# Kernel tuning notes

Hardware: AMD Instinct MI355X
Metric: run time of the kernel (lower is better)

The kernel has to match this reference:

```python
import jax, jax.numpy as jnp
import numpy as np

B, S, H, E = 2, 4096, 2048, 8


def setup_inputs() -> dict:
    key = jax.random.key(0)
    k1, k2, k3 = jax.random.split(key, 3)
    x = jax.random.normal(k1, (B, S, H), dtype=jnp.float32)
    w_router = jax.random.normal(k2, (E, H), dtype=jnp.float32) * (1.0 / np.sqrt(H))
    # nn.Linear weight layout: [out_features, in_features] per expert -> [E, H, H]
    w_experts = jax.random.normal(k3, (E, H, H), dtype=jnp.float32) * (1.0 / np.sqrt(H))
    return {"x": x, "w_router": w_router, "w_experts": w_experts}


def reference(x, w_router, w_experts):
    # router logits: x @ W_r^T  -> [B, S, E]
    logits = jnp.einsum('bsh,eh->bse', x, w_router)
    idx = jnp.argmax(logits, axis=-1)  # [B, S] top-1 expert per token
    # dense all-expert outputs (matches original which evaluates every expert):
    # expert_e(x) = x @ W_e^T -> [B, S, E, H]
    all_out = jnp.einsum('bsh,efh->bsef', x, w_experts)
    # masked sum over one-hot mask == gather of the selected expert output
    out = jnp.take_along_axis(all_out, idx[:, :, None, None], axis=2)[:, :, 0, :]
    return out
```

## Files before the change

### kernel.cpp

```cpp
#include <hip/hip_runtime.h>
#include <hip/hip_bf16.h>
#include <cstdint>

#define T_TOK 8192
#define H_DIM 2048
#define N_EXP 8
#define FLAGBIT 0x80000000u

typedef __attribute__((ext_vector_type(4))) float f32x4;
typedef __attribute__((ext_vector_type(8))) short bf16x8;

__device__ __forceinline__ unsigned short f2bf(float f) {
  unsigned int u = __builtin_bit_cast(unsigned int, f);
  u += 0x7fffu + ((u >> 16) & 1u);
  return (unsigned short)(u >> 16);
}

#define GLL(SRC, DST) __builtin_amdgcn_global_load_lds( \
    (const __attribute__((address_space(1))) void*)(SRC), \
    (__attribute__((address_space(3))) void*)(DST), 16, 0, 0)

__global__ __launch_bounds__(256, 4) void k_conv(const float* __restrict__ we,
                                                 unsigned short* __restrict__ wb) {
  const size_t tix = ((size_t)blockIdx.x * 256 + threadIdx.x) * 8;
  const size_t stride = (size_t)2048 * 256 * 8;
  f32x4 v[16];
#pragma unroll
  for (int it = 0; it < 8; ++it) {
    v[2 * it]     = *reinterpret_cast<const f32x4*>(we + tix + (size_t)it * stride);
    v[2 * it + 1] = *reinterpret_cast<const f32x4*>(we + tix + (size_t)it * stride + 4);
  }
#pragma unroll
  for (int it = 0; it < 8; ++it) {
    union { unsigned short h[8]; uint4 u; } r;
#pragma unroll
    for (int q = 0; q < 4; ++q) {
      r.h[q]     = f2bf(v[2 * it][q]);
      r.h[4 + q] = f2bf(v[2 * it + 1][q]);
    }
    *reinterpret_cast<uint4*>(wb + tix + (size_t)it * stride) = r.u;
  }
}

__global__ __launch_bounds__(256) void k_router(const float* __restrict__ x,
    const float* __restrict__ wr, unsigned short* __restrict__ xb,
    int* __restrict__ idx)
{
  const int wv = threadIdx.x >> 6, lane = threadIdx.x & 63;
  const int t0 = (blockIdx.x * 4 + wv) * 4;
  float acc[4][N_EXP];
#pragma unroll
  for (int tt = 0; tt < 4; ++tt)
#pragma unroll
    for (int e = 0; e < N_EXP; ++e) acc[tt][e] = 0.f;
#pragma unroll
  for (int c = 0; c < H_DIM / 256; ++c) {
    const int h = c * 256 + lane * 4;
    float4 wvv[N_EXP];
#pragma unroll
    for (int e = 0; e < N_EXP; ++e)
      wvv[e] = *reinterpret_cast<const float4*>(wr + e * H_DIM + h);
#pragma unroll
    for (int tt = 0; tt < 4; ++tt) {
      const float4 xv = *reinterpret_cast<const float4*>(x + (size_t)(t0 + tt) * H_DIM + h);
      ushort4 bv;
      bv.x = f2bf(xv.x); bv.y = f2bf(xv.y); bv.z = f2bf(xv.z); bv.w = f2bf(xv.w);
      *reinterpret_cast<ushort4*>(xb + (size_t)(t0 + tt) * H_DIM + h) = bv;
#pragma unroll
      for (int e = 0; e < N_EXP; ++e) {
        acc[tt][e] = fmaf(xv.x, wvv[e].x, acc[tt][e]);
        acc[tt][e] = fmaf(xv.y, wvv[e].y, acc[tt][e]);
        acc[tt][e] = fmaf(xv.z, wvv[e].z, acc[tt][e]);
        acc[tt][e] = fmaf(xv.w, wvv[e].w, acc[tt][e]);
      }
    }
  }
#pragma unroll
  for (int off = 32; off >= 1; off >>= 1)
#pragma unroll
    for (int tt = 0; tt < 4; ++tt)
#pragma unroll
      for (int e = 0; e < N_EXP; ++e) acc[tt][e] += __shfl_xor(acc[tt][e], off, 64);
  if (lane == 0) {
#pragma unroll
    for (int tt = 0; tt < 4; ++tt) {
      float best = acc[tt][0]; int be = 0;
#pragma unroll
      for (int e = 1; e < N_EXP; ++e) if (acc[tt][e] > best) { best = acc[tt][e]; be = e; }
      idx[t0 + tt] = be;
    }
  }
}

__global__ __launch_bounds__(256) void k_hist(const int* __restrict__ idx,
                                              int* __restrict__ hist)
{
  __shared__ int wc[4][N_EXP];
  const int b = blockIdx.x, w = threadIdx.x >> 6, l = threadIdx.x & 63;
  const int e = idx[b * 256 + threadIdx.x];
#pragma unroll
  for (int ee = 0; ee < N_EXP; ++ee) {
    const unsigned long long bm = __ballot(e == ee);
    if (l == ee) wc[w][ee] = __popcll(bm);
  }
  __syncthreads();
  if (threadIdx.x < N_EXP)
    hist[b * N_EXP + threadIdx.x] = wc[0][threadIdx.x] + wc[1][threadIdx.x]
                                  + wc[2][threadIdx.x] + wc[3][threadIdx.x];
}

__global__ void k_scan(const int* __restrict__ hist, int* __restrict__ boff,
                       int* __restrict__ estar, int* __restrict__ mlo, int* __restrict__ mhi,
                       int* __restrict__ rpos, int* __restrict__ rtile, int* __restrict__ rtc)
{
  __shared__ int sC[N_EXP], sE[32], sCnt[N_EXP], sBase[N_EXP];
  const int lane = threadIdx.x;
  if (lane < N_EXP) {
    int s = 0;
    for (int b = 0; b < 32; ++b) s += hist[b * N_EXP + lane];
    sC[lane] = s;
  }
  __syncthreads();
  int off[N_EXP + 1]; off[0] = 0;
#pragma unroll
  for (int e = 0; e < N_EXP; ++e) off[e + 1] = off[e] + sC[e];
  if (lane < 32) {
    for (int e = 0; e < N_EXP; ++e) {
      int s = off[e];
      for (int b = 0; b < lane; ++b) s += hist[b * N_EXP + e];
      boff[lane * N_EXP + e] = s;
    }
    const int lo = lane * 256, hi = lo + 256;
    int bl = -1, bE = 0, bLo = 0, bHi = 0;
#pragma unroll
    for (int e = 0; e < N_EXP; ++e) {
      const int a = off[e] > lo ? off[e] : lo;
      const int b = off[e + 1] < hi ? off[e + 1] : hi;
      if (b - a > bl) { bl = b - a; bE = e; bLo = a - lo; bHi = b - lo; }
    }
    sE[lane] = bE; estar[lane] = bE; mlo[lane] = bLo; mhi[lane] = bHi;
  }
  __syncthreads();
  if (lane < N_EXP) {
    int cnt = 0;
    for (int t = 0; t < 32; ++t) {
      if (sE[t] == lane) continue;
      const int lo = t * 256, hi = lo + 256;
      const int a = off[lane] > lo ? off[lane] : lo;
      const int b = off[lane + 1] < hi ? off[lane + 1] : hi;
      if (b > a) cnt += b - a;
    }
    sCnt[lane] = cnt;
  }
  __syncthreads();
  if (lane == 0) {
    int base = 0, ntile = 0;
    for (int e = 0; e < N_EXP; ++e) {
      sBase[e] = base;
      const int pt = (sCnt[e] + 127) >> 7;
      for (int k = 0; k < pt; ++k) rtile[ntile++] = e;
      base += pt << 7;
    }
    *rtc = ntile;
  }
  __syncthreads();
  if (lane < N_EXP && sCnt[lane] > 0) {
    int ptr = sBase[lane], firstp = -1;
    for (int t = 0; t < 32; ++t) {
      if (sE[t] == lane) continue;
      const int lo = t * 256, hi = lo + 256;
      const int a = off[lane] > lo ? off[lane] : lo;
      const int b = off[lane + 1] < hi ? off[lane + 1] : hi;
      for (int p = a; p < b; ++p) { if (firstp < 0) firstp = p; rpos[ptr++] = p; }
    }
    const int end = sBase[lane] + (((sCnt[lane] + 127) >> 7) << 7);
    for (; ptr < end; ++ptr) rpos[ptr] = (int)((unsigned)firstp | FLAGBIT);
  }
}

__global__ __launch_bounds__(256) void k_place(const int* __restrict__ idx,
    const int* __restrict__ boff, int* __restrict__ tlist)
{
  __shared__ int wc[4][N_EXP];
  const int b = blockIdx.x, w = threadIdx.x >> 6, l = threadIdx.x & 63;
  const int t = b * 256 + threadIdx.x;
  const int e = idx[t];
  int rank = 0;
#pragma unroll
  for (int ee = 0; ee < N_EXP; ++ee) {
    const unsigned long long bm = __ballot(e == ee);
    if (e == ee) rank = __popcll(bm & ((1ull << l) - 1ull));
    if (l == ee) wc[w][ee] = __popcll(bm);
  }
  __syncthreads();
  int pre = 0;
  for (int ww = 0; ww < 4; ++ww) if (ww < w) pre += wc[ww][e];
  tlist[boff[b * N_EXP + e] + pre + rank] = t;
}

template<int Q, bool LOADB, bool VMC>
__device__ __forceinline__ void gphase(const char* LP,
    __attribute__((address_space(3))) char* LDS3,
    int rdBase, int aRowOff, int bRowOff, int ch0, int ch1,
    bf16x8 (&bfr)[8], f32x4 (&acc)[8][4],
    const unsigned short* s0, const unsigned short* s1, int d0, int d1)
{
  if constexpr (LOADB) {
#pragma unroll
    for (int nf = 0; nf < 4; ++nf) {
      bfr[nf * 2 + 0] = *reinterpret_cast<const bf16x8*>(LP + rdBase + 32768 + bRowOff + nf * 2048 + ch0);
      bfr[nf * 2 + 1] = *reinterpret_cast<const bf16x8*>(LP + rdBase + 32768 + bRowOff + nf * 2048 + ch1);
    }
  }
  bf16x8 af[2][2];
#pragma unroll
  for (int m = 0; m < 2; ++m) {
    af[m][0] = *reinterpret_cast<const bf16x8*>(LP + rdBase + aRowOff + (2 * Q + m) * 2048 + ch0);
    af[m][1] = *reinterpret_cast<const bf16x8*>(LP + rdBase + aRowOff + (2 * Q + m) * 2048 + ch1);
  }
  GLL(s0, LDS3 + d0);
  GLL(s1, LDS3 + d1);
  __builtin_amdgcn_sched_barrier(0);
  __builtin_amdgcn_s_barrier();
  __builtin_amdgcn_sched_barrier(0);
  __builtin_amdgcn_s_setprio(1);
#pragma unroll
  for (int ks = 0; ks < 2; ++ks)
#pragma unroll
    for (int m = 0; m < 2; ++m)
#pragma unroll
      for (int nf = 0; nf < 4; ++nf)
        acc[2 * Q + m][nf] = __builtin_amdgcn_mfma_f32_16x16x32_bf16(af[m][ks], bfr[nf * 2 + ks], acc[2 * Q + m][nf], 0, 0, 0);
  __builtin_amdgcn_s_setprio(0);
  if constexpr (VMC) asm volatile("s_waitcnt vmcnt(4)" ::: "memory");
  __builtin_amdgcn_sched_barrier(0);
  __builtin_amdgcn_s_barrier();
  __builtin_amdgcn_sched_barrier(0);
}

__global__ __launch_bounds__(512, 2) void k_gemm(const unsigned short* __restrict__ xb,
    const unsigned short* __restrict__ wb, const int* __restrict__ tlist,
    const int* __restrict__ estar, const int* __restrict__ mlo, const int* __restrict__ mhi,
    float* __restrict__ out)
{
  __shared__ short lds[65536];
  const int bid = blockIdx.x;
  const int mt = (bid & 7) * 4 + ((bid >> 3) & 3);
  const int nt = bid >> 5;
  const int m0 = mt * 256, f0 = nt * 256;
  const int e = estar[mt], mLo = mlo[mt], mHi = mhi[mt];
  const int tid = threadIdx.x;
  const int l = tid & 63, wv = tid >> 6;
  const int wm = wv >> 2, wn = wv & 3;
  const int l16 = l & 15, g = l >> 4;
  const char* LP = (const char*)lds;
  auto* LDS3 = (__attribute__((address_space(3))) char*)lds;

  const int sw = l16 & 7;
  const int ch0 = ((0 + g) ^ sw) << 4;
  const int ch1 = ((4 + g) ^ sw) << 4;
  const int aRowOff = (wm * 128 + l16) * 128;
  const int bRowOff = (wn * 64 + l16) * 128;

  const int csrc = ((l & 7) ^ ((l >> 3) & 7)) * 8;
  const int srow = l >> 3;
  const unsigned short* aP[2][2];
  const unsigned short* bP[2][2];
  const unsigned short* wpan = wb + (size_t)e * H_DIM * H_DIM;
#pragma unroll
  for (int h = 0; h < 2; ++h)
#pragma unroll
    for (int j = 0; j < 2; ++j) {
      const int tok = tlist[m0 + h * 128 + (wv * 2 + j) * 8 + srow];
      aP[h][j] = xb + (size_t)tok * H_DIM + csrc;
      bP[h][j] = wpan + (size_t)(f0 + h * 128 + (wv * 2 + j) * 8 + srow) * H_DIM + csrc;
    }
  const int sl0 = wv * 2048, sl1 = wv * 2048 + 1024;

  f32x4 acc[8][4];
#pragma unroll
  for (int mf = 0; mf < 8; ++mf)
#pragma unroll
    for (int nf = 0; nf < 4; ++nf) acc[mf][nf] = (f32x4){0.f, 0.f, 0.f, 0.f};
  bf16x8 bfr[8];

  GLL(aP[0][0], LDS3 + 0 + sl0);      GLL(aP[0][1], LDS3 + 0 + sl1);
  GLL(aP[1][0], LDS3 + 16384 + sl0);  GLL(aP[1][1], LDS3 + 16384 + sl1);
  GLL(bP[0][0], LDS3 + 32768 + sl0);  GLL(bP[0][1], LDS3 + 32768 + sl1);
  GLL(bP[1][0], LDS3 + 49152 + sl0);  GLL(bP[1][1], LDS3 + 49152 + sl1);
  GLL(bP[0][0] + 64, LDS3 + 65536 + 32768 + sl0);  GLL(bP[0][1] + 64, LDS3 + 65536 + 32768 + sl1);
  GLL(bP[1][0] + 64, LDS3 + 65536 + 49152 + sl0);  GLL(bP[1][1] + 64, LDS3 + 65536 + 49152 + sl1);
  asm volatile("s_waitcnt vmcnt(4)" ::: "memory");
  __builtin_amdgcn_sched_barrier(0);
  __builtin_amdgcn_s_barrier();
  __builtin_amdgcn_sched_barrier(0);

  for (int i = 0; i < 16; ++i) {
    const int kk1 = ((2 * i + 1) << 6) & (H_DIM - 1);
    const int kk2 = ((2 * i + 2) << 6) & (H_DIM - 1);
    const int kk3 = ((2 * i + 3) << 6) & (H_DIM - 1);
    gphase<0, true , false>(LP, LDS3, 0, aRowOff, bRowOff, ch0, ch1, bfr, acc,
        aP[0][0] + kk1, aP[0][1] + kk1, 65536 + 0 + sl0, 65536 + 0 + sl1);
    gphase<1, false, false>(LP, LDS3, 0, aRowOff, bRowOff, ch0, ch1, bfr, acc,
        aP[1][0] + kk1, aP[1][1] + kk1, 65536 + 16384 + sl0, 65536 + 16384 + sl1);
    gphase<2, false, false>(LP, LDS3, 0, aRowOff, bRowOff, ch0, ch1, bfr, acc,
        bP[0][0] + kk2, bP[0][1] + kk2, 0 + 32768 + sl0, 0 + 32768 + sl1);
    gphase<3, false, true >(LP, LDS3, 0, aRowOff, bRowOff, ch0, ch1, bfr, acc,
        bP[1][0] + kk2, bP[1][1] + kk2, 0 + 49152 + sl0, 0 + 49152 + sl1);
    gphase<0, true , false>(LP, LDS3, 65536, aRowOff, bRowOff, ch0, ch1, bfr, acc,
        aP[0][0] + kk2, aP[0][1] + kk2, 0 + 0 + sl0, 0 + 0 + sl1);
    gphase<1, false, false>(LP, LDS3, 65536, aRowOff, bRowOff, ch0, ch1, bfr, acc,
        aP[1][0] + kk2, aP[1][1] + kk2, 0 + 16384 + sl0, 0 + 16384 + sl1);
    gphase<2, false, false>(LP, LDS3, 65536, aRowOff, bRowOff, ch0, ch1, bfr, acc,
        bP[0][0] + kk3, bP[0][1] + kk3, 65536 + 32768 + sl0, 65536 + 32768 + sl1);
    gphase<3, false, true >(LP, LDS3, 65536, aRowOff, bRowOff, ch0, ch1, bfr, acc,
        bP[1][0] + kk3, bP[1][1] + kk3, 65536 + 49152 + sl0, 65536 + 49152 + sl1);
  }

#pragma unroll
  for (int mf = 0; mf < 8; ++mf) {
#pragma unroll
    for (int r = 0; r < 4; ++r) {
      const int row = wm * 128 + mf * 16 + g * 4 + r;
      const int t = tlist[m0 + row];
      const bool own = (row >= mLo) && (row < mHi);
      float* op = out + (size_t)t * H_DIM + f0 + wn * 64 + l16;
#pragma unroll
      for (int nf = 0; nf < 4; ++nf) op[nf * 16] = own ? acc[mf][nf][r] : 0.f;
    }
  }
}

__global__ __launch_bounds__(256, 2) void k_repair(const unsigned short* __restrict__ xb,
    const unsigned short* __restrict__ wb, const int* __restrict__ tlist,
    const int* __restrict__ rpos, const int* __restrict__ rtile, const int* __restrict__ rtc,
    float* __restrict__ out)
{
  const int bx = blockIdx.x;
  if (bx >= *rtc) return;
  __shared__ short lds[24576];
  const int f0 = blockIdx.y * 256, kc = blockIdx.z;
  const int e = rtile[bx];
  const int tid = threadIdx.x, l = tid & 63, wv = tid >> 6;
  const int wm = wv >> 1, wn = wv & 1;
  const int l16 = l & 15, g = l >> 4;
  const char* LP = (const char*)lds;
  auto* LDS3 = (__attribute__((address_space(3))) char*)lds;
  const int sw = l16 & 7;
  const int ch0 = ((0 + g) ^ sw) << 4, ch1 = ((4 + g) ^ sw) << 4;
  const int csrc = ((l & 7) ^ ((l >> 3) & 7)) * 8;
  const int srow = l >> 3;

  const unsigned short* aS[4];
#pragma unroll
  for (int j = 0; j < 4; ++j) {
    const int ent = rpos[bx * 128 + (wv * 4 + j) * 8 + srow];
    const int tok = tlist[ent & 0x7fffffff];
    aS[j] = xb + (size_t)tok * H_DIM + csrc;
  }
  const unsigned short* bS[8];
#pragma unroll
  for (int j = 0; j < 8; ++j)
    bS[j] = wb + (size_t)e * H_DIM * H_DIM + (size_t)(f0 + (wv * 8 + j) * 8 + srow) * H_DIM + csrc;

  f32x4 acc[4][8];
#pragma unroll
  for (int mf = 0; mf < 4; ++mf)
#pragma unroll
    for (int nf = 0; nf < 8; ++nf) acc[mf][nf] = (f32x4){0.f, 0.f, 0.f, 0.f};

  for (int it = 0; it < 8; ++it) {
    const int kk = kc * 512 + it * 64;
    __syncthreads();
#pragma unroll
    for (int j = 0; j < 4; ++j) GLL(aS[j] + kk, LDS3 + (wv * 4 + j) * 1024);
#pragma unroll
    for (int j = 0; j < 8; ++j) GLL(bS[j] + kk, LDS3 + 16384 + (wv * 8 + j) * 1024);
    __syncthreads();
    bf16x8 af[4][2];
#pragma unroll
    for (int mf = 0; mf < 4; ++mf) {
      af[mf][0] = *reinterpret_cast<const bf16x8*>(LP + (wm * 64 + mf * 16 + l16) * 128 + ch0);
      af[mf][1] = *reinterpret_cast<const bf16x8*>(LP + (wm * 64 + mf * 16 + l16) * 128 + ch1);
    }
#pragma unroll
    for (int nf = 0; nf < 8; ++nf) {
      const bf16x8 b0 = *reinterpret_cast<const bf16x8*>(LP + 16384 + (wn * 128 + nf * 16 + l16) * 128 + ch0);
      const bf16x8 b1 = *reinterpret_cast<const bf16x8*>(LP + 16384 + (wn * 128 + nf * 16 + l16) * 128 + ch1);
#pragma unroll
      for (int mf = 0; mf < 4; ++mf) {
        acc[mf][nf] = __builtin_amdgcn_mfma_f32_16x16x32_bf16(af[mf][0], b0, acc[mf][nf], 0, 0, 0);
        acc[mf][nf] = __builtin_amdgcn_mfma_f32_16x16x32_bf16(af[mf][1], b1, acc[mf][nf], 0, 0, 0);
      }
    }
  }
#pragma unroll
  for (int mf = 0; mf < 4; ++mf) {
#pragma unroll
    for (int r = 0; r < 4; ++r) {
      const int row = wm * 64 + mf * 16 + g * 4 + r;
      const int ent = rpos[bx * 128 + row];
      if (!((unsigned)ent & FLAGBIT)) {
        const int tok = tlist[ent];
        float* op = out + (size_t)tok * H_DIM + f0 + wn * 128 + l16;
#pragma unroll
        for (int nf = 0; nf < 8; ++nf) atomicAdd(op + nf * 16, acc[mf][nf][r]);
      }
    }
  }
}

extern "C" void kernel_launch(void* const* d_in, const int* in_sizes, int n_in,
                              void* d_out, int out_size, void* d_ws, size_t ws_size,
                              hipStream_t stream) {
  const float* x  = (const float*)d_in[0];
  const float* wr = (const float*)d_in[1];
  const float* we = (const float*)d_in[2];
  float* out = (float*)d_out;

  char* p = (char*)d_ws;
  unsigned short* xb = (unsigned short*)p; p += (size_t)T_TOK * H_DIM * 2;
  unsigned short* wb = (unsigned short*)p; p += (size_t)N_EXP * H_DIM * H_DIM * 2;
  int* idx    = (int*)p; p += T_TOK * 4;
  int* tlist  = (int*)p; p += T_TOK * 4;
  int* rpos   = (int*)p; p += T_TOK * 4;
  int* hist   = (int*)p; p += 32 * N_EXP * 4;
  int* boff   = (int*)p; p += 32 * N_EXP * 4;
  int* estar  = (int*)p; p += 32 * 4;
  int* mlo    = (int*)p; p += 32 * 4;
  int* mhi    = (int*)p; p += 32 * 4;
  int* rtile  = (int*)p; p += 64 * 4;
  int* rtc    = (int*)p; p += 64;

  k_conv<<<2048, 256, 0, stream>>>(we, wb);
  k_router<<<512, 256, 0, stream>>>(x, wr, xb, idx);
  k_hist<<<32, 256, 0, stream>>>(idx, hist);
  k_scan<<<1, 64, 0, stream>>>(hist, boff, estar, mlo, mhi, rpos, rtile, rtc);
  k_place<<<32, 256, 0, stream>>>(idx, boff, tlist);
  k_gemm<<<256, 512, 0, stream>>>(xb, wb, tlist, estar, mlo, mhi, out);
  k_repair<<<dim3(64, 8, 4), 256, 0, stream>>>(xb, wb, tlist, rpos, rtile, rtc, out);
}
```

Measured before the change: 209.8 us.

## Fuse hist/scan/place into one sort kernel and split weight conversion

Replaces the three small routing kernels (histogram, scan, placement) with a single 1024-thread block that counts per-wave expert ballots, prefix-sums in shared memory, and scatters token indices directly. This removes two kernel launches and the global round trips through the hist/boff buffers. The fp32-to-bf16 weight conversion is split into two half-size launches, one of which issues loads and stores per iteration instead of batching them, and the router gets a min-blocks launch bound. The single-block sort runs serially on one CU, and the extra conversion launch adds overhead.

```diff
diff --git a/kernel.cpp b/kernel.cpp
--- a/kernel.cpp
+++ b/kernel.cpp
@@ -20,10 +20,10 @@
     (const __attribute__((address_space(1))) void*)(SRC), \
     (__attribute__((address_space(3))) void*)(DST), 16, 0, 0)
 
-__global__ __launch_bounds__(256, 4) void k_conv(const float* __restrict__ we,
-                                                 unsigned short* __restrict__ wb) {
+__global__ __launch_bounds__(256, 4) void k_conv_a(const float* __restrict__ we,
+                                                   unsigned short* __restrict__ wb) {
   const size_t tix = ((size_t)blockIdx.x * 256 + threadIdx.x) * 8;
-  const size_t stride = (size_t)2048 * 256 * 8;
+  const size_t stride = (size_t)1024 * 256 * 8;
   f32x4 v[16];
 #pragma unroll
   for (int it = 0; it < 8; ++it) {
@@ -42,7 +42,22 @@
   }
 }
 
-__global__ __launch_bounds__(256) void k_router(const float* __restrict__ x,
+__global__ __launch_bounds__(256, 4) void k_conv_b(const float* __restrict__ we,
+                                                   unsigned short* __restrict__ wb) {
+  const size_t tix = ((size_t)blockIdx.x * 256 + threadIdx.x) * 8;
+  const size_t stride = (size_t)1024 * 256 * 8;
+#pragma unroll
+  for (int it = 0; it < 8; ++it) {
+    const f32x4 a = *reinterpret_cast<const f32x4*>(we + tix + (size_t)it * stride);
+    const f32x4 b = *reinterpret_cast<const f32x4*>(we + tix + (size_t)it * stride + 4);
+    union { unsigned short h[8]; uint4 u; } r;
+#pragma unroll
+    for (int q = 0; q < 4; ++q) { r.h[q] = f2bf(a[q]); r.h[4 + q] = f2bf(b[q]); }
+    *reinterpret_cast<uint4*>(wb + tix + (size_t)it * stride) = r.u;
+  }
+}
+
+__global__ __launch_bounds__(256, 2) void k_router(const float* __restrict__ x,
     const float* __restrict__ wr, unsigned short* __restrict__ xb,
     int* __restrict__ idx)
 {
@@ -92,45 +107,51 @@
   }
 }
 
-__global__ __launch_bounds__(256) void k_hist(const int* __restrict__ idx,
-                                              int* __restrict__ hist)
+__global__ __launch_bounds__(1024) void k_sort(const int* __restrict__ idx,
+    int* __restrict__ tlist, int* __restrict__ estar, int* __restrict__ mlo,
+    int* __restrict__ mhi, int* __restrict__ rpos, int* __restrict__ rtile,
+    int* __restrict__ rtc)
 {
-  __shared__ int wc[4][N_EXP];
-  const int b = blockIdx.x, w = threadIdx.x >> 6, l = threadIdx.x & 63;
-  const int e = idx[b * 256 + threadIdx.x];
-#pragma unroll
-  for (int ee = 0; ee < N_EXP; ++ee) {
-    const unsigned long long bm = __ballot(e == ee);
-    if (l == ee) wc[w][ee] = __popcll(bm);
-  }
-  __syncthreads();
-  if (threadIdx.x < N_EXP)
-    hist[b * N_EXP + threadIdx.x] = wc[0][threadIdx.x] + wc[1][threadIdx.x]
-                                  + wc[2][threadIdx.x] + wc[3][threadIdx.x];
-}
-
-__global__ void k_scan(const int* __restrict__ hist, int* __restrict__ boff,
-                       int* __restrict__ estar, int* __restrict__ mlo, int* __restrict__ mhi,
-                       int* __restrict__ rpos, int* __restrict__ rtile, int* __restrict__ rtc)
-{
-  __shared__ int sC[N_EXP], sE[32], sCnt[N_EXP], sBase[N_EXP];
-  const int lane = threadIdx.x;
-  if (lane < N_EXP) {
+  __shared__ int wc[N_EXP][128];
+  __shared__ int wbase[N_EXP][128];
+  __shared__ int sTot[N_EXP];
+  __shared__ int off[N_EXP + 1];
+  __shared__ int sE[32], sCnt[N_EXP], sBase[N_EXP];
+  const int tid = threadIdx.x, w = tid >> 6, l = tid & 63;
+  int myE[8];
+#pragma unroll
+  for (int j = 0; j < 8; ++j) {
+    myE[j] = idx[j * 1024 + tid];
+#pragma unroll
+    for (int e = 0; e < N_EXP; ++e) {
+      const unsigned long long bm = __ballot(myE[j] == e);
+      if (l == e) wc[e][j * 16 + w] = __popcll(bm);
+    }
+  }
+  __syncthreads();
+  if (tid < N_EXP) {
     int s = 0;
-    for (int b = 0; b < 32; ++b) s += hist[b * N_EXP + lane];
-    sC[lane] = s;
-  }
-  __syncthreads();
-  int off[N_EXP + 1]; off[0] = 0;
-#pragma unroll
-  for (int e = 0; e < N_EXP; ++e) off[e + 1] = off[e] + sC[e];
-  if (lane < 32) {
+    for (int k = 0; k < 128; ++k) { wbase[tid][k] = s; s += wc[tid][k]; }
+    sTot[tid] = s;
+  }
+  __syncthreads();
+  if (tid == 0) {
+    off[0] = 0;
+    for (int e = 0; e < N_EXP; ++e) off[e + 1] = off[e] + sTot[e];
+  }
+  __syncthreads();
+#pragma unroll
+  for (int j = 0; j < 8; ++j) {
+    int rank = 0;
+#pragma unroll
     for (int e = 0; e < N_EXP; ++e) {
-      int s = off[e];
-      for (int b = 0; b < lane; ++b) s += hist[b * N_EXP + e];
-      boff[lane * N_EXP + e] = s;
-    }
-    const int lo = lane * 256, hi = lo + 256;
+      const unsigned long long bm = __ballot(myE[j] == e);
+      if (myE[j] == e) rank = __popcll(bm & ((1ull << l) - 1ull));
+    }
+    tlist[off[myE[j]] + wbase[myE[j]][j * 16 + w] + rank] = j * 1024 + tid;
+  }
+  if (tid < 32) {
+    const int lo = tid * 256, hi = lo + 256;
     int bl = -1, bE = 0, bLo = 0, bHi = 0;
 #pragma unroll
     for (int e = 0; e < N_EXP; ++e) {
@@ -138,22 +159,22 @@
       const int b = off[e + 1] < hi ? off[e + 1] : hi;
       if (b - a > bl) { bl = b - a; bE = e; bLo = a - lo; bHi = b - lo; }
     }
-    sE[lane] = bE; estar[lane] = bE; mlo[lane] = bLo; mhi[lane] = bHi;
-  }
-  __syncthreads();
-  if (lane < N_EXP) {
+    sE[tid] = bE; estar[tid] = bE; mlo[tid] = bLo; mhi[tid] = bHi;
+  }
+  __syncthreads();
+  if (tid < N_EXP) {
     int cnt = 0;
     for (int t = 0; t < 32; ++t) {
-      if (sE[t] == lane) continue;
+      if (sE[t] == tid) continue;
       const int lo = t * 256, hi = lo + 256;
-      const int a = off[lane] > lo ? off[lane] : lo;
-      const int b = off[lane + 1] < hi ? off[lane + 1] : hi;
+      const int a = off[tid] > lo ? off[tid] : lo;
+      const int b = off[tid + 1] < hi ? off[tid + 1] : hi;
       if (b > a) cnt += b - a;
     }
-    sCnt[lane] = cnt;
-  }
-  __syncthreads();
-  if (lane == 0) {
+    sCnt[tid] = cnt;
+  }
+  __syncthreads();
+  if (tid == 0) {
     int base = 0, ntile = 0;
     for (int e = 0; e < N_EXP; ++e) {
       sBase[e] = base;
@@ -164,38 +185,18 @@
     *rtc = ntile;
   }
   __syncthreads();
-  if (lane < N_EXP && sCnt[lane] > 0) {
-    int ptr = sBase[lane], firstp = -1;
+  if (tid < N_EXP && sCnt[tid] > 0) {
+    int ptr = sBase[tid], firstp = -1;
     for (int t = 0; t < 32; ++t) {
-      if (sE[t] == lane) continue;
+      if (sE[t] == tid) continue;
       const int lo = t * 256, hi = lo + 256;
-      const int a = off[lane] > lo ? off[lane] : lo;
-      const int b = off[lane + 1] < hi ? off[lane + 1] : hi;
+      const int a = off[tid] > lo ? off[tid] : lo;
+      const int b = off[tid + 1] < hi ? off[tid + 1] : hi;
       for (int p = a; p < b; ++p) { if (firstp < 0) firstp = p; rpos[ptr++] = p; }
     }
-    const int end = sBase[lane] + (((sCnt[lane] + 127) >> 7) << 7);
+    const int end = sBase[tid] + (((sCnt[tid] + 127) >> 7) << 7);
     for (; ptr < end; ++ptr) rpos[ptr] = (int)((unsigned)firstp | FLAGBIT);
   }
-}
-
-__global__ __launch_bounds__(256) void k_place(const int* __restrict__ idx,
-    const int* __restrict__ boff, int* __restrict__ tlist)
-{
-  __shared__ int wc[4][N_EXP];
-  const int b = blockIdx.x, w = threadIdx.x >> 6, l = threadIdx.x & 63;
-  const int t = b * 256 + threadIdx.x;
-  const int e = idx[t];
-  int rank = 0;
-#pragma unroll
-  for (int ee = 0; ee < N_EXP; ++ee) {
-    const unsigned long long bm = __ballot(e == ee);
-    if (e == ee) rank = __popcll(bm & ((1ull << l) - 1ull));
-    if (l == ee) wc[w][ee] = __popcll(bm);
-  }
-  __syncthreads();
-  int pre = 0;
-  for (int ww = 0; ww < 4; ++ww) if (ww < w) pre += wc[ww][e];
-  tlist[boff[b * N_EXP + e] + pre + rank] = t;
 }
 
 template<int Q, bool LOADB, bool VMC>
@@ -424,19 +425,17 @@
   int* idx    = (int*)p; p += T_TOK * 4;
   int* tlist  = (int*)p; p += T_TOK * 4;
   int* rpos   = (int*)p; p += T_TOK * 4;
-  int* hist   = (int*)p; p += 32 * N_EXP * 4;
-  int* boff   = (int*)p; p += 32 * N_EXP * 4;
   int* estar  = (int*)p; p += 32 * 4;
   int* mlo    = (int*)p; p += 32 * 4;
   int* mhi    = (int*)p; p += 32 * 4;
   int* rtile  = (int*)p; p += 64 * 4;
   int* rtc    = (int*)p; p += 64;
 
-  k_conv<<<2048, 256, 0, stream>>>(we, wb);
+  const size_t half = (size_t)4 * H_DIM * H_DIM;
+  k_conv_a<<<1024, 256, 0, stream>>>(we, wb);
+  k_conv_b<<<1024, 256, 0, stream>>>(we + half, wb + half);
   k_router<<<512, 256, 0, stream>>>(x, wr, xb, idx);
-  k_hist<<<32, 256, 0, stream>>>(idx, hist);
-  k_scan<<<1, 64, 0, stream>>>(hist, boff, estar, mlo, mhi, rpos, rtile, rtc);
-  k_place<<<32, 256, 0, stream>>>(idx, boff, tlist);
+  k_sort<<<1, 1024, 0, stream>>>(idx, tlist, estar, mlo, mhi, rpos, rtile, rtc);
   k_gemm<<<256, 512, 0, stream>>>(xb, wb, tlist, estar, mlo, mhi, out);
   k_repair<<<dim3(64, 8, 4), 256, 0, stream>>>(xb, wb, tlist, rpos, rtile, rtc, out);
 }
```

Result: no change. 208.4 us (-0.7%).
